# Kernel tuning notes

Measured on AMD Instinct MI355X. Metric: run time of the kernel, lower is better.

The kernel has to match this reference:

```python
import jax, jax.numpy as jnp
import numpy as np

B, L, D, K, C = 4, 1024, 1024, 20, 21  # images, proposals/img, feat dim, dict size, classes


def setup_inputs() -> dict:
    key = jax.random.key(0)
    ks = jax.random.split(key, 6)
    return {
        "x": jax.random.normal(ks[0], (B, L, D), jnp.float32),
        "dic": jax.random.normal(ks[1], (K, D), jnp.float32),
        "prior": jax.random.uniform(ks[2], (K,), jnp.float32),
        "Wy_w": jax.random.normal(ks[3], (C, D), jnp.float32) * 0.02,
        "Wy_b": jnp.zeros((C,), jnp.float32),
        "Wz_w": jax.random.normal(ks[4], (C, D), jnp.float32) * 0.02,
        "Wz_b": jnp.zeros((C,), jnp.float32),
        "cs_w": jax.random.normal(ks[5], (C, 2 * D), jnp.float32) * 0.01,
        "cs_b": jnp.zeros((C,), jnp.float32),
    }


def reference(x, dic, prior, Wy_w, Wy_b, Wz_w, Wz_b, cs_w, cs_b):
    # attention over a small class dictionary, then pairwise outer-sum causal logits.
    scale = 1.0 / jnp.sqrt(jnp.asarray(C, x.dtype))  # embedding_size ** 0.5 == sqrt(21)
    zd = dic @ Wz_w.T + Wz_b  # [K, C] Wz(dic), shared across images

    def per_image(y):  # y: [L, D]
        att = jax.nn.softmax(((y @ Wy_w.T + Wy_b) @ zd.T) * scale, axis=1)  # [L, K]
        # prior @ (att[:, :, None] * dic[None]) == (att * prior) @ dic
        z = (att * prior[None, :]) @ dic  # [L, D]
        # causal_score(cat(y_i, z_j)) == y_i @ W[:, :D].T + z_j @ W[:, D:].T + b
        ly = y @ cs_w[:, :D].T            # [L, C]
        lz = z @ cs_w[:, D:].T + cs_b     # [L, C]
        return (ly[:, None, :] + lz[None, :, :]).reshape(L * L, C)  # [L*L, C]

    return jax.vmap(per_image)(x)  # [B, L*L, C]
```

## Files before the change

### kernel.cpp

```cpp
#include <hip/hip_runtime.h>
#include <math.h>

#define BB 4
#define LL 1024
#define DD 1024
#define KK 20
#define CC 21
#define LC (LL * CC)
#define NQ (LC / 4)
#define XSTRIDE 1032

typedef float vf4    __attribute__((ext_vector_type(4)));
typedef short bf16x8 __attribute__((ext_vector_type(8)));
typedef float f32x4  __attribute__((ext_vector_type(4)));

__device__ __forceinline__ unsigned short f2bf(float f) {
    unsigned int u = __builtin_bit_cast(unsigned int, f);
    u += 0x7FFFu + ((u >> 16) & 1u);
    return (unsigned short)(u >> 16);
}

__device__ __forceinline__ float wave_reduce_sum(float v) {
    #pragma unroll
    for (int off = 1; off < 64; off <<= 1)
        v += __shfl_xor(v, off, 64);
    return v;
}

__global__ __launch_bounds__(64) void k0_zdM(
    const float* __restrict__ dic,
    const float* __restrict__ Wz_w, const float* __restrict__ Wz_b,
    const float* __restrict__ cs_w, const float* __restrict__ Wy_w,
    float* __restrict__ zd, float* __restrict__ M,
    unsigned short* __restrict__ Wcat)
{
    int blk = blockIdx.x;
    int lane = threadIdx.x;

    if (blk < 2 * KK * CC) {
        bool isM = (blk >= KK * CC);
        int e2 = isM ? blk - KK * CC : blk;
        int k = e2 / CC, c = e2 % CC;
        const float* a = dic + k * DD;
        const float* w = isM ? (cs_w + (size_t)c * (2 * DD) + DD) : (Wz_w + c * DD);
        float p = 0.f;
        #pragma unroll
        for (int i = 0; i < DD / 64; ++i) {
            int d = lane + 64 * i;
            p += a[d] * w[d];
        }
        p = wave_reduce_sum(p);
        if (lane == 0) {
            if (isM) M[e2] = p;
            else     zd[e2] = p + Wz_b[c];
        }
    } else {
        int e2 = blk - 2 * KK * CC;
        int base = e2 * 2048;
        #pragma unroll
        for (int t = 0; t < 32; ++t) {
            int i = base + lane + 64 * t;
            int c = i >> 10, k = i & 1023;
            float v;
            if (c < CC)          v = Wy_w[(size_t)c * DD + k];
            else if (c < 2 * CC) v = cs_w[(size_t)(c - CC) * (2 * DD) + k];
            else                 v = 0.f;
            Wcat[i] = f2bf(v);
        }
    }
}

__global__ __launch_bounds__(512) void k1_mfma(
    const float* __restrict__ x,
    const float* __restrict__ prior,
    const float* __restrict__ Wy_b, const float* __restrict__ cs_b,
    const unsigned short* __restrict__ Wcat,
    const float* __restrict__ zd, const float* __restrict__ M,
    float* __restrict__ ly_ws, float* __restrict__ lz_ws)
{
    const int tid  = threadIdx.x;
    const int wid  = tid >> 6;
    const int lane = tid & 63;
    const int fr   = lane & 15;
    const int kg   = lane >> 4;
    const int r0   = blockIdx.x * 16;

    __shared__ float zds[KK * CC];
    __shared__ float Ms[KK * CC];
    __shared__ float pr[KK];
    __shared__ float bias[2 * CC];
    __shared__ float pacc[8 * 16 * 49];
    __shared__ unsigned short xT[16 * XSTRIDE];

    for (int i = tid; i < KK * CC; i += 512) { zds[i] = zd[i]; Ms[i] = M[i]; }
    if (tid < KK) pr[tid] = prior[tid];
    if (tid < CC) { bias[tid] = Wy_b[tid]; bias[CC + tid] = cs_b[tid]; }

    #pragma unroll
    for (int i = 0; i < 8; ++i) {
        int f = tid + i * 512;
        int row  = f >> 8;
        int col4 = f & 255;
        float4 v = *reinterpret_cast<const float4*>(x + (size_t)(r0 + row) * DD + col4 * 4);
        unsigned int lo = (unsigned int)f2bf(v.x) | ((unsigned int)f2bf(v.y) << 16);
        unsigned int hi = (unsigned int)f2bf(v.z) | ((unsigned int)f2bf(v.w) << 16);
        *reinterpret_cast<uint2*>(&xT[row * XSTRIDE + col4 * 4]) = make_uint2(lo, hi);
    }
    __syncthreads();

    const int kbase = wid * 128;
    const unsigned short* w0p = Wcat + (size_t)(fr +  0) * DD + kbase + kg * 8;
    const unsigned short* w1p = Wcat + (size_t)(fr + 16) * DD + kbase + kg * 8;
    const unsigned short* w2p = Wcat + (size_t)(fr + 32) * DD + kbase + kg * 8;
    const unsigned short* ap  = xT + fr * XSTRIDE + kbase + kg * 8;

    f32x4 acc0 = {0.f, 0.f, 0.f, 0.f};
    f32x4 acc1 = {0.f, 0.f, 0.f, 0.f};
    f32x4 acc2 = {0.f, 0.f, 0.f, 0.f};

    #pragma unroll
    for (int ks = 0; ks < 4; ++ks) {
        bf16x8 af = *reinterpret_cast<const bf16x8*>(ap + ks * 32);
        bf16x8 b0 = *reinterpret_cast<const bf16x8*>(w0p + ks * 32);
        bf16x8 b1 = *reinterpret_cast<const bf16x8*>(w1p + ks * 32);
        bf16x8 b2 = *reinterpret_cast<const bf16x8*>(w2p + ks * 32);
        acc0 = __builtin_amdgcn_mfma_f32_16x16x32_bf16(af, b0, acc0, 0, 0, 0);
        acc1 = __builtin_amdgcn_mfma_f32_16x16x32_bf16(af, b1, acc1, 0, 0, 0);
        acc2 = __builtin_amdgcn_mfma_f32_16x16x32_bf16(af, b2, acc2, 0, 0, 0);
    }

    #pragma unroll
    for (int j = 0; j < 4; ++j) {
        float* pw = pacc + ((wid * 16) + kg * 4 + j) * 49;
        pw[fr]      = acc0[j];
        pw[16 + fr] = acc1[j];
        pw[32 + fr] = acc2[j];
    }
    __syncthreads();

    #pragma unroll
    for (int p = 0; p < 2; ++p) {
        int o = tid + p * 512;
        if (o < 768) {
            int row = o / 48, col = o % 48;
            float s = 0.f;
            #pragma unroll
            for (int w = 0; w < 8; ++w) s += pacc[((w * 16) + row) * 49 + col];
            pacc[row * 49 + col] = s;
        }
    }
    __syncthreads();

    if (tid < 64) {
        const float* f = pacc + fr * 49;
        const float scale = 0.21821789023599238f;
        float s[KK];
        float m = -1e30f;
        #pragma unroll
        for (int k = 0; k < KK; ++k) {
            float t = 0.f;
            #pragma unroll
            for (int c = 0; c < CC; ++c) t += (f[c] + bias[c]) * zds[k * CC + c];
            s[k] = t * scale;
            m = fmaxf(m, s[k]);
        }
        float sum = 0.f;
        #pragma unroll
        for (int k = 0; k < KK; ++k) { s[k] = expf(s[k] - m); sum += s[k]; }
        float inv = 1.f / sum;
        float wk[KK];
        #pragma unroll
        for (int k = 0; k < KK; ++k) wk[k] = s[k] * inv * pr[k];

        size_t rr = (size_t)(r0 + fr);
        for (int c = kg; c < CC; c += 4) {
            float lzv = bias[CC + c];
            #pragma unroll
            for (int k = 0; k < KK; ++k) lzv += wk[k] * Ms[k * CC + c];
            ly_ws[rr * CC + c] = f[CC + c];
            lz_ws[rr * CC + c] = lzv;
        }
    }
}

__global__ __launch_bounds__(512) void k2_outer(
    const float* __restrict__ ly_ws, const float* __restrict__ lz_ws,
    float* __restrict__ out)
{
    int tid = threadIdx.x;
    int blk = blockIdx.x;
    int b  = blk >> 8;
    int i0 = (blk & 255) << 2;

    __shared__ vf4 lyp4[4 * CC];
    {
        float* lyp = reinterpret_cast<float*>(lyp4);
        if (tid < 4 * 84) {
            int i = tid / 84, f = tid % 84;
            lyp[i * 84 + f] = ly_ws[(size_t)(b * LL + i0 + i) * CC + (f % 21)];
        }
    }
    const float* lzp = lz_ws + (size_t)b * LC;
    vf4 lzv[11];
    #pragma unroll
    for (int it = 0; it < 11; ++it) {
        int idx = tid + it * 512;
        lzv[it] = (idx < NQ) ? *reinterpret_cast<const vf4*>(lzp + (size_t)idx * 4)
                             : (vf4){0.f, 0.f, 0.f, 0.f};
    }
    __syncthreads();
    int g0 = tid % 21;

    #pragma unroll
    for (int i = 0; i < 4; ++i) {
        float* op = out + (size_t)(b * LL + i0 + i) * LC;
        const vf4* lyp_i = lyp4 + i * CC;
        int g = g0;
        #pragma unroll
        for (int it = 0; it < 11; ++it) {
            int idx = tid + it * 512;
            if (idx < NQ) {
                *reinterpret_cast<vf4*>(op + (size_t)idx * 4) = lzv[it] + lyp_i[g];
            }
            g += 8; if (g >= 21) g -= 21;
        }
    }
}

extern "C" void kernel_launch(void* const* d_in, const int* in_sizes, int n_in,
                              void* d_out, int out_size, void* d_ws, size_t ws_size,
                              hipStream_t stream)
{
    const float* x     = (const float*)d_in[0];
    const float* dic   = (const float*)d_in[1];
    const float* prior = (const float*)d_in[2];
    const float* Wy_w  = (const float*)d_in[3];
    const float* Wy_b  = (const float*)d_in[4];
    const float* Wz_w  = (const float*)d_in[5];
    const float* Wz_b  = (const float*)d_in[6];
    const float* cs_w  = (const float*)d_in[7];
    const float* cs_b  = (const float*)d_in[8];
    float* out = (float*)d_out;

    float* ws = (float*)d_ws;
    float* zd = ws;
    float* M  = ws + 512;
    float* ly = ws + 1024;
    float* lz = ly + BB * LL * CC;
    unsigned short* Wcat = (unsigned short*)(ws + 1024 + 2 * BB * LL * CC);

    k0_zdM <<<dim3(2 * KK * CC + 24), dim3(64),  0, stream>>>(dic, Wz_w, Wz_b, cs_w, Wy_w,
                                                              zd, M, Wcat);
    k1_mfma<<<dim3(BB * LL / 16),     dim3(512), 0, stream>>>(x, prior, Wy_b, cs_b, Wcat,
                                                              zd, M, ly, lz);
    k2_outer<<<dim3(BB * LL / 4),     dim3(512), 0, stream>>>(ly, lz, out);
}
```

Baseline: 99.54 us.

## Shrink k1 row tile to 8 rows with 4 waves; vectorize k0 dot products

The projection kernel now processes 8 rows per block with 256 threads, and each wave covers 256 of the K dimension instead of 128. This doubles the block count and cuts the cross-wave partial-sum reduction from 8 waves to 4. The MFMA A operand duplicates rows 0-7 into lanes 8-15, so half of the MFMA output is wasted. The k0 dot products now use float4 loads. Most of the runtime is in the 344MB output write of k2, so the effect on total time is probably small.

```diff
diff --git a/kernel.cpp b/kernel.cpp
--- a/kernel.cpp
+++ b/kernel.cpp
@@ -8,7 +8,7 @@
 #define CC 21
 #define LC (LL * CC)
 #define NQ (LC / 4)
-#define XSTRIDE 1032
+#define XS 1032
 
 typedef float vf4    __attribute__((ext_vector_type(4)));
 typedef short bf16x8 __attribute__((ext_vector_type(8)));
@@ -26,6 +26,8 @@
         v += __shfl_xor(v, off, 64);
     return v;
 }
+
+#define DOT4(a, b) ((a).x*(b).x + (a).y*(b).y + (a).z*(b).z + (a).w*(b).w)
 
 __global__ __launch_bounds__(64) void k0_zdM(
     const float* __restrict__ dic,
@@ -41,13 +43,15 @@
         bool isM = (blk >= KK * CC);
         int e2 = isM ? blk - KK * CC : blk;
         int k = e2 / CC, c = e2 % CC;
-        const float* a = dic + k * DD;
-        const float* w = isM ? (cs_w + (size_t)c * (2 * DD) + DD) : (Wz_w + c * DD);
+        const float4* a4 = reinterpret_cast<const float4*>(dic + (size_t)k * DD);
+        const float*  w  = isM ? (cs_w + (size_t)c * (2 * DD) + DD) : (Wz_w + (size_t)c * DD);
+        const float4* w4 = reinterpret_cast<const float4*>(w);
         float p = 0.f;
         #pragma unroll
-        for (int i = 0; i < DD / 64; ++i) {
-            int d = lane + 64 * i;
-            p += a[d] * w[d];
+        for (int i = 0; i < 4; ++i) {
+            float4 av = a4[lane + 64 * i];
+            float4 wv = w4[lane + 64 * i];
+            p += DOT4(av, wv);
         }
         p = wave_reduce_sum(p);
         if (lane == 0) {
@@ -70,7 +74,7 @@
     }
 }
 
-__global__ __launch_bounds__(512) void k1_mfma(
+__global__ __launch_bounds__(256) void k1_mfma(
     const float* __restrict__ x,
     const float* __restrict__ prior,
     const float* __restrict__ Wy_b, const float* __restrict__ cs_b,
@@ -82,44 +86,45 @@
     const int wid  = tid >> 6;
     const int lane = tid & 63;
     const int fr   = lane & 15;
+    const int frm  = fr & 7;
     const int kg   = lane >> 4;
-    const int r0   = blockIdx.x * 16;
+    const int r0   = blockIdx.x * 8;
 
     __shared__ float zds[KK * CC];
     __shared__ float Ms[KK * CC];
     __shared__ float pr[KK];
     __shared__ float bias[2 * CC];
-    __shared__ float pacc[8 * 16 * 49];
-    __shared__ unsigned short xT[16 * XSTRIDE];
-
-    for (int i = tid; i < KK * CC; i += 512) { zds[i] = zd[i]; Ms[i] = M[i]; }
+    __shared__ unsigned short xT[8 * XS];
+    __shared__ float pacc[4 * 8 * 49];
+
+    for (int i = tid; i < KK * CC; i += 256) { zds[i] = zd[i]; Ms[i] = M[i]; }
     if (tid < KK) pr[tid] = prior[tid];
     if (tid < CC) { bias[tid] = Wy_b[tid]; bias[CC + tid] = cs_b[tid]; }
 
     #pragma unroll
     for (int i = 0; i < 8; ++i) {
-        int f = tid + i * 512;
+        int f = tid + i * 256;
         int row  = f >> 8;
         int col4 = f & 255;
         float4 v = *reinterpret_cast<const float4*>(x + (size_t)(r0 + row) * DD + col4 * 4);
         unsigned int lo = (unsigned int)f2bf(v.x) | ((unsigned int)f2bf(v.y) << 16);
         unsigned int hi = (unsigned int)f2bf(v.z) | ((unsigned int)f2bf(v.w) << 16);
-        *reinterpret_cast<uint2*>(&xT[row * XSTRIDE + col4 * 4]) = make_uint2(lo, hi);
-    }
-    __syncthreads();
-
-    const int kbase = wid * 128;
+        *reinterpret_cast<uint2*>(&xT[row * XS + col4 * 4]) = make_uint2(lo, hi);
+    }
+    __syncthreads();
+
+    const int kbase = wid * 256;
     const unsigned short* w0p = Wcat + (size_t)(fr +  0) * DD + kbase + kg * 8;
     const unsigned short* w1p = Wcat + (size_t)(fr + 16) * DD + kbase + kg * 8;
     const unsigned short* w2p = Wcat + (size_t)(fr + 32) * DD + kbase + kg * 8;
-    const unsigned short* ap  = xT + fr * XSTRIDE + kbase + kg * 8;
+    const unsigned short* ap  = &xT[frm * XS + kbase + kg * 8];
 
     f32x4 acc0 = {0.f, 0.f, 0.f, 0.f};
     f32x4 acc1 = {0.f, 0.f, 0.f, 0.f};
     f32x4 acc2 = {0.f, 0.f, 0.f, 0.f};
 
     #pragma unroll
-    for (int ks = 0; ks < 4; ++ks) {
+    for (int ks = 0; ks < 8; ++ks) {
         bf16x8 af = *reinterpret_cast<const bf16x8*>(ap + ks * 32);
         bf16x8 b0 = *reinterpret_cast<const bf16x8*>(w0p + ks * 32);
         bf16x8 b1 = *reinterpret_cast<const bf16x8*>(w1p + ks * 32);
@@ -129,30 +134,31 @@
         acc2 = __builtin_amdgcn_mfma_f32_16x16x32_bf16(af, b2, acc2, 0, 0, 0);
     }
 
-    #pragma unroll
-    for (int j = 0; j < 4; ++j) {
-        float* pw = pacc + ((wid * 16) + kg * 4 + j) * 49;
-        pw[fr]      = acc0[j];
-        pw[16 + fr] = acc1[j];
-        pw[32 + fr] = acc2[j];
-    }
-    __syncthreads();
-
-    #pragma unroll
-    for (int p = 0; p < 2; ++p) {
-        int o = tid + p * 512;
-        if (o < 768) {
-            int row = o / 48, col = o % 48;
-            float s = 0.f;
-            #pragma unroll
-            for (int w = 0; w < 8; ++w) s += pacc[((w * 16) + row) * 49 + col];
-            pacc[row * 49 + col] = s;
-        }
+    if (kg < 2) {
+        #pragma unroll
+        for (int j = 0; j < 4; ++j) {
+            float* pw = pacc + ((wid * 8) + kg * 4 + j) * 49;
+            pw[fr]      = acc0[j];
+            pw[16 + fr] = acc1[j];
+            pw[32 + fr] = acc2[j];
+        }
+    }
+    __syncthreads();
+
+    for (int o = tid; o < 384; o += 256) {
+        int row = o / 48, col = o % 48;
+        float s = pacc[row * 49 + col]
+                + pacc[(8  + row) * 49 + col]
+                + pacc[(16 + row) * 49 + col]
+                + pacc[(24 + row) * 49 + col];
+        pacc[row * 49 + col] = s;
     }
     __syncthreads();
 
     if (tid < 64) {
-        const float* f = pacc + fr * 49;
+        const int r = tid & 7;
+        const int g = tid >> 3;
+        const float* f = pacc + r * 49;
         const float scale = 0.21821789023599238f;
         float s[KK];
         float m = -1e30f;
@@ -172,8 +178,8 @@
         #pragma unroll
         for (int k = 0; k < KK; ++k) wk[k] = s[k] * inv * pr[k];
 
-        size_t rr = (size_t)(r0 + fr);
-        for (int c = kg; c < CC; c += 4) {
+        size_t rr = (size_t)(r0 + r);
+        for (int c = g; c < CC; c += 8) {
             float lzv = bias[CC + c];
             #pragma unroll
             for (int k = 0; k < KK; ++k) lzv += wk[k] * Ms[k * CC + c];
@@ -251,7 +257,7 @@
 
     k0_zdM <<<dim3(2 * KK * CC + 24), dim3(64),  0, stream>>>(dic, Wz_w, Wz_b, cs_w, Wy_w,
                                                               zd, M, Wcat);
-    k1_mfma<<<dim3(BB * LL / 16),     dim3(512), 0, stream>>>(x, prior, Wy_b, cs_b, Wcat,
+    k1_mfma<<<dim3(BB * LL / 8),      dim3(256), 0, stream>>>(x, prior, Wy_b, cs_b, Wcat,
                                                               zd, M, ly, lz);
     k2_outer<<<dim3(BB * LL / 4),     dim3(512), 0, stream>>>(ly, lz, out);
 }
```

After: 101.5 us. About the same (+2.0%).
